# Optimization experiments

Hardware: AMD Instinct MI355X
Metric: run time of the kernel (lower is better)

Reference implementation:

```python
import jax, jax.numpy as jnp
import numpy as np

D_MODEL = 1024
D_STATE = 16
D_CONV = 4
EXPAND = 2
D_INNER = EXPAND * D_MODEL          # 2048
DT_RANK = (D_MODEL + 15) // 16      # 64
BSZ, T0, H0, W0 = 4, 8, 16, 16
SEQLEN = T0 * H0 * W0               # 2048
N_BANDS = 8


def setup_inputs() -> dict:
    key = jax.random.key(0)
    ks = jax.random.split(key, 8)
    hidden_states = jax.random.normal(ks[0], (BSZ, SEQLEN, D_MODEL), jnp.float32)
    in_proj_w = jax.random.normal(ks[1], (2 * D_INNER, D_MODEL), jnp.float32) * (D_MODEL ** -0.5)
    conv_w = jax.random.normal(ks[2], (D_INNER, 1, D_CONV), jnp.float32) * (D_CONV ** -0.5)
    conv_b = jnp.zeros((D_INNER,), jnp.float32)
    x_proj_w = jax.random.normal(ks[3], (DT_RANK + 2 * D_STATE, D_INNER), jnp.float32) * (D_INNER ** -0.5)
    dt_std = DT_RANK ** -0.5
    dt_proj_w = jax.random.uniform(ks[4], (D_INNER, DT_RANK), jnp.float32, -dt_std, dt_std)
    # inverse-softplus init of dt bias, as in the torch module
    dt = jnp.exp(jax.random.uniform(ks[5], (D_INNER,), jnp.float32)
                 * (np.log(0.1) - np.log(0.001)) + np.log(0.001))
    dt = jnp.clip(dt, 1e-4, None)
    dt_proj_b = dt + jnp.log(-jnp.expm1(-dt))
    A_log = jnp.log(jnp.tile(jnp.arange(1, D_STATE + 1, dtype=jnp.float32)[None, :], (D_INNER, 1)))
    D_param = jnp.ones((D_INNER,), jnp.float32)
    out_proj_w = jax.random.normal(ks[6], (D_MODEL, D_INNER), jnp.float32) * (D_INNER ** -0.5)
    return dict(hidden_states=hidden_states, T=T0, H=H0, W=W0,
                in_proj_w=in_proj_w, conv_w=conv_w, conv_b=conv_b,
                x_proj_w=x_proj_w, dt_proj_w=dt_proj_w, dt_proj_b=dt_proj_b,
                A_log=A_log, D=D_param, out_proj_w=out_proj_w)


def _channel_alignment(x, B, T, H, W):
    """x: (B, C, L=T*H*W) -> (align_loss scalar, features (B*T, C))."""
    C = x.shape[1]
    x4 = x.reshape(B, C, T, H, W).transpose(0, 2, 1, 3, 4).reshape(B * T, C, H, W)
    fr = jnp.fft.rfft2(x4, axes=(-2, -1))
    mag = jnp.sqrt(fr.real ** 2 + fr.imag ** 2 + 1e-8)
    mag = jnp.fft.fftshift(mag, axes=(-2, -1))
    Wr = mag.shape[-1]                      # W//2 + 1
    hg = jnp.arange(H)[:, None]
    wg = jnp.arange(Wr)[None, :]
    r = jnp.sqrt(((hg - H // 2) / H) ** 2 + ((wg - Wr // 2) / Wr) ** 2)
    masks = jnp.stack([((r >= i / N_BANDS) & (r < (i + 1) / N_BANDS)).astype(mag.dtype)
                       for i in range(N_BANDS)])          # (8, H, Wr)
    bands = jnp.einsum('bchw,khw->bck', mag, masks)        # (B*T, C, 8)
    bands = bands / (bands.sum(-1, keepdims=True) + 1e-8)
    features = bands[..., N_BANDS // 2:].sum(-1)           # (B*T, C) high-freq ratio
    fn = features / jnp.maximum(jnp.linalg.norm(features, axis=1, keepdims=True), 1e-12)
    sim = fn @ fn.T
    Bt = features.shape[0]
    loss = 1.0 - sim.sum() / (Bt * Bt)
    return loss, features


def _invert_A(A_log, features):
    """Blend A_log toward its column-flipped version, weighted by channel features."""
    A_max = A_log.max(axis=0, keepdims=True)
    A_min = A_log.min(axis=0, keepdims=True)
    A_flipped = A_max + A_min - A_log
    attention = jnp.linalg.norm(jnp.exp(A_log), axis=1)
    attention = attention / (attention.max() + 1e-8)
    f = jax.nn.softmax(jax.lax.stop_gradient(features).mean(axis=0))
    alpha = jnp.clip(f * (1.0 - attention), 0.0, 1.0)[:, None]   # (d_inner, 1)
    return (1.0 - alpha) * A_log + alpha * A_flipped


def reference(hidden_states, T, H, W, in_proj_w, conv_w, conv_b,
              x_proj_w, dt_proj_w, dt_proj_b, A_log, D, out_proj_w):
    B, L, _ = hidden_states.shape
    xz = jnp.einsum('bld,ed->bel', hidden_states, in_proj_w)      # (B, 2*d_inner, L)
    x, z = xz[:, :D_INNER], xz[:, D_INNER:]

    align_loss, features = _channel_alignment(x, B, T, H, W)
    A_log_new = _invert_A(A_log, features)
    A = -jnp.exp(A_log_new)                                       # (d_inner, d_state)

    # causal depthwise conv1d + SiLU (left pad d_conv-1 == torch pad then slice :L)
    xc = jax.lax.conv_general_dilated(x, conv_w, (1,), [(D_CONV - 1, 0)],
                                      dimension_numbers=('NCH', 'OIH', 'NCH'),
                                      feature_group_count=D_INNER)
    xc = jax.nn.silu(xc + conv_b[None, :, None])                  # (B, d_inner, L)

    x_dbl = jnp.einsum('bdl,ed->ble', xc, x_proj_w)               # (B, L, dt_rank+2N)
    dt_low = x_dbl[..., :DT_RANK]
    Bm = x_dbl[..., DT_RANK:DT_RANK + D_STATE]                    # (B, L, N)
    Cm = x_dbl[..., DT_RANK + D_STATE:]                           # (B, L, N)
    delta = jax.nn.softplus(jnp.einsum('blr,dr->bld', dt_low, dt_proj_w) + dt_proj_b)

    u = xc.transpose(0, 2, 1)                                     # (B, L, d_inner)

    def step(s, inp):
        d_t, u_t, B_t, C_t = inp                                  # (B,D),(B,D),(B,N),(B,N)
        s = s * jnp.exp(d_t[..., None] * A) + (d_t * u_t)[..., None] * B_t[:, None, :]
        y_t = jnp.einsum('bdn,bn->bd', s, C_t)
        return s, y_t

    s0 = jnp.zeros((B, D_INNER, D_STATE), delta.dtype)
    _, ys = jax.lax.scan(step, s0,
                         (delta.transpose(1, 0, 2), u.transpose(1, 0, 2),
                          Bm.transpose(1, 0, 2), Cm.transpose(1, 0, 2)))
    y = ys.transpose(1, 0, 2)                                     # (B, L, d_inner)
    y = y + u * D
    y = y * jax.nn.silu(z.transpose(0, 2, 1))
    out = jnp.einsum('bld,ed->ble', y, out_proj_w)                # (B, L, d_model)
    return out, align_loss
```

## Files before the change

kernel.cpp:

```cpp
#include <hip/hip_runtime.h>
#include <math.h>
#include <stdint.h>

#define LSEQ 2048
#define DM   1024
#define DI   2048
#define NC   32
#define CL   64

#define OFF_X     ((size_t)0)
#define OFF_Z     ((size_t)16777216)
#define OFF_U     ((size_t)33554432)
#define OFF_S     ((size_t)50331648)
#define OFF_CS    (OFF_S)
#define OFF_SDT   (OFF_S + 4194304)
#define OFF_XDBL  (OFF_S + 4456448)
#define OFF_FEAT  (OFF_S + 5242880)
#define OFF_AWS   (OFF_S + 5308448)
#define OFF_B1    ((size_t)58720256)

__device__ __forceinline__ float silu_(float x) { return x / (1.f + __expf(-x)); }
__device__ __forceinline__ float softplus_(float x) {
  return fmaxf(x, 0.f) + log1pf(__expf(-fabsf(x)));
}
__device__ __forceinline__ unsigned short f2bf(float x) {
  unsigned int u = __float_as_uint(x);
  u += 0x7fffu + ((u >> 16) & 1u);
  return (unsigned short)(u >> 16);
}
__device__ __forceinline__ float bf2f(unsigned short h) {
  return __uint_as_float(((unsigned int)h) << 16);
}

typedef __attribute__((ext_vector_type(8))) short bf16x8;
typedef __attribute__((ext_vector_type(4))) float f32x4;

__device__ __forceinline__ void gl2lds16(const void* g, void* l) {
  __builtin_amdgcn_global_load_lds(
      (const __attribute__((address_space(1))) unsigned int*)(uintptr_t)g,
      (__attribute__((address_space(3))) unsigned int*)(uintptr_t)l,
      16, 0, 0);
}

#define BARRIER_()                                   \
  do {                                               \
    asm volatile("" ::: "memory");                   \
    __builtin_amdgcn_s_barrier();                    \
    asm volatile("" ::: "memory");                   \
  } while (0)

__global__ __launch_bounds__(256) void split2_w(
    const float* __restrict__ a, unsigned short* __restrict__ oa, int ksa,
    size_t na4,
    const float* __restrict__ b, unsigned short* __restrict__ ob, int ksb)
{
  size_t i4 = ((size_t)blockIdx.x << 8) + threadIdx.x;
  const float* src; unsigned short* dst; int ks;
  if (i4 < na4) { src = a; dst = oa; ks = ksa; }
  else          { src = b; dst = ob; ks = ksb; i4 -= na4; }
  const size_t flat = i4 << 2;
  const int K = 1 << ks;
  const size_t row = flat >> ks;
  const int k = (int)(flat & (size_t)(K - 1));
  float4 v = *(const float4*)(src + flat);
  float f[4] = {v.x, v.y, v.z, v.w};
  unsigned short h[4], lo[4];
#pragma unroll
  for (int c = 0; c < 4; ++c) { h[c] = f2bf(f[c]); lo[c] = f2bf(f[c] - bf2f(h[c])); }
  unsigned short* o = dst + (row << (ks + 1)) + k;
  *(uint2*)(o)     = make_uint2((unsigned)h[0]  | ((unsigned)h[1]  << 16),
                                (unsigned)h[2]  | ((unsigned)h[3]  << 16));
  *(uint2*)(o + K) = make_uint2((unsigned)lo[0] | ((unsigned)lo[1] << 16),
                                (unsigned)lo[2] | ((unsigned)lo[3] << 16));
}

template <int NPASS, int MH, int NH>
__device__ __forceinline__ void phase_mfma(
    const unsigned short* __restrict__ shc, f32x4 (&acc)[8][4],
    int wm, int wn, int lm, int roff)
{
  bf16x8 aH[4], bH[2], aL[4], bL[2];
#pragma unroll
  for (int ii = 0; ii < 4; ++ii) {
    const int ar = (wm + (MH * 4 + ii) * 16 + lm) * 32 + roff;
    aH[ii] = *(const bf16x8*)(shc + ar);
    if constexpr (NPASS > 1) aL[ii] = *(const bf16x8*)(shc + 2 * 8192 + ar);
  }
#pragma unroll
  for (int jj = 0; jj < 2; ++jj) {
    const int br = (wn + (NH * 2 + jj) * 16 + lm) * 32 + roff;
    bH[jj] = *(const bf16x8*)(shc + 8192 + br);
    if constexpr (NPASS > 1) bL[jj] = *(const bf16x8*)(shc + 3 * 8192 + br);
  }
  __builtin_amdgcn_s_setprio(1);
#pragma unroll
  for (int ii = 0; ii < 4; ++ii)
#pragma unroll
    for (int jj = 0; jj < 2; ++jj) {
      const int i = MH * 4 + ii, j = NH * 2 + jj;
      acc[i][j] = __builtin_amdgcn_mfma_f32_16x16x32_bf16(aH[ii], bH[jj], acc[i][j], 0, 0, 0);
      if constexpr (NPASS > 1) {
        acc[i][j] = __builtin_amdgcn_mfma_f32_16x16x32_bf16(aH[ii], bL[jj], acc[i][j], 0, 0, 0);
        acc[i][j] = __builtin_amdgcn_mfma_f32_16x16x32_bf16(aL[ii], bH[jj], acc[i][j], 0, 0, 0);
      }
    }
  __builtin_amdgcn_s_setprio(0);
}

template <int NPASS>
__global__ __launch_bounds__(512, 2) void gemm_8ph(
    const unsigned short* __restrict__ Ap, const unsigned short* __restrict__ Bp,
    float* __restrict__ C, int K, int ldc)
{
  constexpr int NTEN = (NPASS > 1) ? 4 : 2;
  __shared__ unsigned short sh[2][NTEN][256 * 32];
  const int tid = threadIdx.x;
  const int bn = blockIdx.x << 8;
  const int bm = blockIdx.y << 8;
  const int K2 = K * 2;
  const int wave = tid >> 6, lane = tid & 63;
  const int wm = (wave >> 2) << 7;
  const int wn = (wave & 3) << 6;
  const int lm = lane & 15, quad = lane >> 4;
  const int roff = ((quad ^ ((lm >> 1) & 3)) << 3);

  const int r0 = tid >> 2;
  const int kq = (((tid & 3) ^ ((r0 >> 1) & 3)) << 3);
  const unsigned short* a0 = Ap + (size_t)(bm + r0) * K2 + kq;
  const unsigned short* a1 = a0 + (size_t)128 * K2;
  const unsigned short* b0 = Bp + (size_t)(bn + r0) * K2 + kq;
  const unsigned short* b1 = b0 + (size_t)128 * K2;
  const int ls0 = tid * 8, ls1 = 4096 + tid * 8;

  f32x4 acc[8][4] = {};
  const int NT = K >> 5;

  {
    unsigned short* s = &sh[0][0][0];
    gl2lds16(a0, s + ls0);
    gl2lds16(a1, s + ls1);
    if constexpr (NPASS > 1) {
      gl2lds16(a0 + K, s + 2 * 8192 + ls0);
      gl2lds16(a1 + K, s + 2 * 8192 + ls1);
    }
    gl2lds16(b0, s + 8192 + ls0);
    gl2lds16(b1, s + 8192 + ls1);
    if constexpr (NPASS > 1) {
      gl2lds16(b0 + K, s + 3 * 8192 + ls0);
      gl2lds16(b1 + K, s + 3 * 8192 + ls1);
    }
  }

  for (int t = 0; t < NT - 1; ++t) {
    const unsigned short* cur = &sh[t & 1][0][0];
    unsigned short* nxt = &sh[(t + 1) & 1][0][0];
    const int kn = (t + 1) << 5;

    gl2lds16(a0 + kn, nxt + ls0);
    gl2lds16(a1 + kn, nxt + ls1);
    if constexpr (NPASS > 1) {
      gl2lds16(a0 + K + kn, nxt + 2 * 8192 + ls0);
      gl2lds16(a1 + K + kn, nxt + 2 * 8192 + ls1);
      asm volatile("s_waitcnt vmcnt(4)" ::: "memory");
    } else {
      asm volatile("s_waitcnt vmcnt(2)" ::: "memory");
    }
    BARRIER_();
    phase_mfma<NPASS, 0, 0>(cur, acc, wm, wn, lm, roff);
    BARRIER_();
    gl2lds16(b0 + kn, nxt + 8192 + ls0);
    gl2lds16(b1 + kn, nxt + 8192 + ls1);
    if constexpr (NPASS > 1) {
      gl2lds16(b0 + K + kn, nxt + 3 * 8192 + ls0);
      gl2lds16(b1 + K + kn, nxt + 3 * 8192 + ls1);
    }
    phase_mfma<NPASS, 0, 1>(cur, acc, wm, wn, lm, roff);
    BARRIER_();
    phase_mfma<NPASS, 1, 0>(cur, acc, wm, wn, lm, roff);
    BARRIER_();
    phase_mfma<NPASS, 1, 1>(cur, acc, wm, wn, lm, roff);
    BARRIER_();
  }

  {
    const unsigned short* cur = &sh[(NT - 1) & 1][0][0];
    asm volatile("s_waitcnt vmcnt(0)" ::: "memory");
    BARRIER_();
    phase_mfma<NPASS, 0, 0>(cur, acc, wm, wn, lm, roff);
    BARRIER_();
    phase_mfma<NPASS, 0, 1>(cur, acc, wm, wn, lm, roff);
    BARRIER_();
    phase_mfma<NPASS, 1, 0>(cur, acc, wm, wn, lm, roff);
    BARRIER_();
    phase_mfma<NPASS, 1, 1>(cur, acc, wm, wn, lm, roff);
  }

#pragma unroll
  for (int i = 0; i < 8; ++i) {
    const int m = bm + wm + i * 16 + quad * 4;
#pragma unroll
    for (int j = 0; j < 4; ++j) {
      const int n = bn + wn + j * 16 + lm;
#pragma unroll
      for (int r = 0; r < 4; ++r)
        C[(size_t)(m + r) * ldc + n] = acc[i][j][r];
    }
  }
}

template <int NPASS, int A_PACKED>
__global__ __launch_bounds__(256) void gemm_mfma(
    const void* __restrict__ Avp, const unsigned short* __restrict__ Bp,
    float* __restrict__ C, int K, int ldc, int nxs)
{
  __shared__ unsigned short AsH[128 * 32];
  __shared__ unsigned short BsH[128 * 32];
  __shared__ unsigned short AsL[(NPASS > 1) ? 128 * 32 : 8];
  __shared__ unsigned short BsL[(NPASS > 1) ? 128 * 32 : 8];
  const int tid = threadIdx.x;
  const int lin = blockIdx.y * gridDim.x + blockIdx.x;
  const int xcd = lin & 7;
  const int t = lin >> 3;
  const int nmask = (1 << nxs) - 1;
  const int bn = (((t & nmask) << 3) | xcd) << 7;
  const int bm = (t >> nxs) << 7;
  const int K2 = K * 2;

  const int wave = tid >> 6, lane = tid & 63;
  const int wm = (wave >> 1) << 6, wn = (wave & 1) << 6;
  const int lm = lane & 15, quad = lane >> 4;
  const int sw = (lm >> 1) & 3;

  f32x4 acc[4][4] = {};

  const int r0 = tid >> 2;
  const int kq = ((tid & 3) ^ ((r0 >> 1) & 3)) << 3;
  const unsigned short* BgH0 = Bp + (size_t)(bn + r0) * K2 + kq;
  const unsigned short* BgH1 = Bp + (size_t)(bn + 64 + r0) * K2 + kq;
  unsigned short* lA0 = &AsH[(size_t)tid * 8];
  unsigned short* lA1 = &AsH[(size_t)(256 + tid) * 8];
  unsigned short* lB0 = &BsH[(size_t)tid * 8];
  unsigned short* lB1 = &BsH[(size_t)(256 + tid) * 8];
  unsigned short* lAl0 = (NPASS > 1) ? &AsL[(size_t)tid * 8] : nullptr;
  unsigned short* lAl1 = (NPASS > 1) ? &AsL[(size_t)(256 + tid) * 8] : nullptr;
  unsigned short* lBl0 = (NPASS > 1) ? &BsL[(size_t)tid * 8] : nullptr;
  unsigned short* lBl1 = (NPASS > 1) ? &BsL[(size_t)(256 + tid) * 8] : nullptr;

  const unsigned short* AgH0 = nullptr; const unsigned short* AgH1 = nullptr;
  const unsigned int* Apk0 = nullptr; const unsigned int* Apk1 = nullptr;
  if (A_PACKED) {
    const unsigned int* Au = (const unsigned int*)Avp;
    Apk0 = Au + (size_t)(bm + r0) * K + kq;
    Apk1 = Au + (size_t)(bm + 64 + r0) * K + kq;
  } else {
    const unsigned short* Ab = (const unsigned short*)Avp;
    AgH0 = Ab + (size_t)(bm + r0) * K2 + kq;
    AgH1 = Ab + (size_t)(bm + 64 + r0) * K2 + kq;
  }

  for (int k0 = 0; k0 < K; k0 += 32) {
    __syncthreads();
    if (A_PACKED) {
      uint4 u0 = *(const uint4*)(Apk0 + k0);
      uint4 u1 = *(const uint4*)(Apk0 + k0 + 4);
      uint4 v0 = *(const uint4*)(Apk1 + k0);
      uint4 v1 = *(const uint4*)(Apk1 + k0 + 4);
      unsigned p[8] = {u0.x, u0.y, u0.z, u0.w, u1.x, u1.y, u1.z, u1.w};
      unsigned q[8] = {v0.x, v0.y, v0.z, v0.w, v1.x, v1.y, v1.z, v1.w};
      unsigned hu[4], lu[4], hv[4], lv[4];
#pragma unroll
      for (int c = 0; c < 4; ++c) {
        hu[c] = (p[2*c] & 0xffffu) | (p[2*c+1] << 16);
        lu[c] = (p[2*c] >> 16)     | (p[2*c+1] & 0xffff0000u);
        hv[c] = (q[2*c] & 0xffffu) | (q[2*c+1] << 16);
        lv[c] = (q[2*c] >> 16)     | (q[2*c+1] & 0xffff0000u);
      }
      *(uint4*)lA0  = make_uint4(hu[0], hu[1], hu[2], hu[3]);
      *(uint4*)lA1  = make_uint4(hv[0], hv[1], hv[2], hv[3]);
      if (NPASS > 1) {
        *(uint4*)lAl0 = make_uint4(lu[0], lu[1], lu[2], lu[3]);
        *(uint4*)lAl1 = make_uint4(lv[0], lv[1], lv[2], lv[3]);
      }
    } else {
      gl2lds16(AgH0 + k0, lA0);
      gl2lds16(AgH1 + k0, lA1);
      if (NPASS > 1) {
        gl2lds16(AgH0 + K + k0, lAl0);
        gl2lds16(AgH1 + K + k0, lAl1);
      }
    }
    gl2lds16(BgH0 + k0, lB0);
    gl2lds16(BgH1 + k0, lB1);
    if (NPASS > 1) {
      gl2lds16(BgH0 + K + k0, lBl0);
      gl2lds16(BgH1 + K + k0, lBl1);
    }
    __syncthreads();

    bf16x8 aH[4], bH[4];
#pragma unroll
    for (int i = 0; i < 4; ++i)
      aH[i] = *(const bf16x8*)&AsH[(wm + i * 16 + lm) * 32 + ((quad ^ sw) << 3)];
#pragma unroll
    for (int j = 0; j < 4; ++j)
      bH[j] = *(const bf16x8*)&BsH[(wn + j * 16 + lm) * 32 + ((quad ^ sw) << 3)];
#pragma unroll
    for (int i = 0; i < 4; ++i)
#pragma unroll
      for (int j = 0; j < 4; ++j)
        acc[i][j] = __builtin_amdgcn_mfma_f32_16x16x32_bf16(aH[i], bH[j], acc[i][j], 0, 0, 0);
    if (NPASS > 1) {
      bf16x8 aL[4], bL[4];
#pragma unroll
      for (int i = 0; i < 4; ++i)
        aL[i] = *(const bf16x8*)&AsL[(wm + i * 16 + lm) * 32 + ((quad ^ sw) << 3)];
#pragma unroll
      for (int j = 0; j < 4; ++j)
        bL[j] = *(const bf16x8*)&BsL[(wn + j * 16 + lm) * 32 + ((quad ^ sw) << 3)];
#pragma unroll
      for (int i = 0; i < 4; ++i)
#pragma unroll
        for (int j = 0; j < 4; ++j) {
          acc[i][j] = __builtin_amdgcn_mfma_f32_16x16x32_bf16(aH[i], bL[j], acc[i][j], 0, 0, 0);
          acc[i][j] = __builtin_amdgcn_mfma_f32_16x16x32_bf16(aL[i], bH[j], acc[i][j], 0, 0, 0);
        }
    }
  }

#pragma unroll
  for (int i = 0; i < 4; ++i) {
    const int m = bm + wm + i * 16 + quad * 4;
#pragma unroll
    for (int j = 0; j < 4; ++j) {
      const int n = bn + wn + j * 16 + lm;
#pragma unroll
      for (int r = 0; r < 4; ++r)
        C[(size_t)(m + r) * ldc + n] = acc[i][j][r];
    }
  }
}

template <int EPI>
__global__ __launch_bounds__(256) void gemm_nt(
    const float* __restrict__ A, int lda,
    const float* __restrict__ B, int ldb,
    float* __restrict__ C, int ldc,
    int N, int K, const float* __restrict__ bias, size_t cseg)
{
  __shared__ float As[16][68];
  __shared__ float Bs[16][68];
  const int tid = threadIdx.x;
  const int bm = blockIdx.y << 6;
  const int bn = blockIdx.x << 6;
  const int kz = blockIdx.z;
  A += (size_t)kz * K;
  B += (size_t)kz * K;
  C += (size_t)kz * cseg;
  const int lr = tid >> 2;
  const int lk = (tid & 3) << 2;
  const int tx = tid & 15, ty = tid >> 4;

  float acc[4][4];
#pragma unroll
  for (int i = 0; i < 4; ++i)
#pragma unroll
    for (int j = 0; j < 4; ++j) acc[i][j] = 0.f;

  const float* Apt = A + (size_t)(bm + lr) * lda + lk;
  const float* Bpt = B + (size_t)(bn + lr) * ldb + lk;
  const bool bv = (bn + lr) < N;

  for (int k0 = 0; k0 < K; k0 += 16) {
    float4 a4 = *(const float4*)(Apt + k0);
    float4 b4 = bv ? *(const float4*)(Bpt + k0) : make_float4(0.f, 0.f, 0.f, 0.f);
    __syncthreads();
    As[lk + 0][lr] = a4.x; As[lk + 1][lr] = a4.y;
    As[lk + 2][lr] = a4.z; As[lk + 3][lr] = a4.w;
    Bs[lk + 0][lr] = b4.x; Bs[lk + 1][lr] = b4.y;
    Bs[lk + 2][lr] = b4.z; Bs[lk + 3][lr] = b4.w;
    __syncthreads();
#pragma unroll
    for (int k = 0; k < 16; ++k) {
      const float4 av = *(const float4*)(&As[k][ty << 2]);
      const float4 bw = *(const float4*)(&Bs[k][tx << 2]);
      float a4r[4] = {av.x, av.y, av.z, av.w};
      float b4r[4] = {bw.x, bw.y, bw.z, bw.w};
#pragma unroll
      for (int i = 0; i < 4; ++i)
#pragma unroll
        for (int j = 0; j < 4; ++j)
          acc[i][j] = fmaf(a4r[i], b4r[j], acc[i][j]);
    }
  }

  const int m = bm + (ty << 2);
  const int n = bn + (tx << 2);
#pragma unroll
  for (int i = 0; i < 4; ++i) {
    float v[4] = {acc[i][0], acc[i][1], acc[i][2], acc[i][3]};
    if (EPI == 1) {
#pragma unroll
      for (int j = 0; j < 4; ++j)
        if (n + j < N) v[j] = softplus_(v[j] + bias[n + j]);
    }
    if (n + 3 < N) {
      *(float4*)(C + (size_t)(m + i) * ldc + n) = make_float4(v[0], v[1], v[2], v[3]);
    } else {
#pragma unroll
      for (int j = 0; j < 4; ++j)
        if (n + j < N) C[(size_t)(m + i) * ldc + n + j] = v[j];
    }
  }
}

__global__ __launch_bounds__(256) void reduce4(
    const float* __restrict__ P, float* __restrict__ O, size_t seg)
{
  const size_t i = ((size_t)blockIdx.x << 8) + threadIdx.x;
  float4 a = ((const float4*)P)[i];
  float4 b = ((const float4*)(P + seg))[i];
  float4 c = ((const float4*)(P + 2 * seg))[i];
  float4 d = ((const float4*)(P + 3 * seg))[i];
  ((float4*)O)[i] = make_float4(a.x + b.x + c.x + d.x,
                                a.y + b.y + c.y + d.y,
                                a.z + b.z + c.z + d.z,
                                a.w + b.w + c.w + d.w);
}

__global__ __launch_bounds__(256) void feat_kernel(
    const float* __restrict__ X, float* __restrict__ features)
{
  __shared__ float xin[256][17];
  __shared__ float Rf[16 * 315];
  __shared__ float tc[16], ts[16];
  __shared__ float part2[16][16][2];

  const int tid = threadIdx.x;
  const int frame = blockIdx.x >> 7;
  const int cg = blockIdx.x & 127;
  const int b = frame >> 3, t = frame & 7;
  const int c0 = cg << 4;

  if (tid < 16) {
    float ang = 0.39269908169872414f * (float)tid;
    tc[tid] = cosf(ang);
    ts[tid] = sinf(ang);
  }
  const float* xb = X + ((size_t)(b * LSEQ + t * 256) << 11) + c0;
  for (int i = tid; i < 256 * 16; i += 256) {
    int hw = i >> 4, ci = i & 15;
    xin[hw][ci] = xb[((size_t)hw << 11) + ci];
  }
  __syncthreads();

  {
    const int ci = tid & 15, h = tid >> 4;
    float re[9], im[9];
#pragma unroll
    for (int kw = 0; kw < 9; ++kw) { re[kw] = 0.f; im[kw] = 0.f; }
#pragma unroll
    for (int w = 0; w < 16; ++w) {
      float x = xin[(h << 4) + w][ci];
#pragma unroll
      for (int kw = 0; kw < 9; ++kw) {
        int ph = (kw * w) & 15;
        re[kw] = fmaf(x, tc[ph], re[kw]);
        im[kw] = fmaf(-x, ts[ph], im[kw]);
      }
    }
#pragma unroll
    for (int kw = 0; kw < 9; ++kw) {
      Rf[ci * 315 + kw * 35 + 2 * h]     = re[kw];
      Rf[ci * 315 + kw * 35 + 2 * h + 1] = im[kw];
    }
  }
  __syncthreads();

  {
    const int ci = tid & 15, kh = tid >> 4;
    float ut = 0.f, tt = 0.f;
    for (int kw = 0; kw < 9; ++kw) {
      float fre = 0.f, fim = 0.f;
#pragma unroll
      for (int h = 0; h < 16; ++h) {
        int ph = (kh * h) & 15;
        float c = tc[ph], s = ts[ph];
        float rr = Rf[ci * 315 + kw * 35 + 2 * h];
        float ri = Rf[ci * 315 + kw * 35 + 2 * h + 1];
        fre += rr * c + ri * s;
        fim += ri * c - rr * s;
      }
      float mag = sqrtf(fre * fre + fim * fim + 1e-8f);
      int sh = (kh + 8) & 15;
      int sw2 = kw + 4; if (sw2 >= 9) sw2 -= 9;
      float dh = (float)(sh - 8) / 16.0f;
      float dw = (float)(sw2 - 4) / 9.0f;
      tt += mag;
      if (dh * dh + dw * dw >= 0.25f) ut += mag;
    }
    part2[ci][kh][0] = ut;
    part2[ci][kh][1] = tt;
  }
  __syncthreads();

  if (tid < 16) {
    float ut = 0.f, tt = 0.f;
    for (int kh = 0; kh < 16; ++kh) { ut += part2[tid][kh][0]; tt += part2[tid][kh][1]; }
    features[frame * DI + c0 + tid] = ut / (tt + 1e-8f);
  }
}

__global__ __launch_bounds__(256) void alpha_kernel(
    const float* __restrict__ feats, const float* __restrict__ A_log,
    float* __restrict__ Aws, float* __restrict__ loss_out)
{
  __shared__ float red[256];
  __shared__ float invn[32];
  __shared__ float PT[32][257];
  __shared__ float AM[256][17];
  __shared__ float sAmax[16], sAmin[16];
  const int tid = threadIdx.x;

  float pn[32];
#pragma unroll
  for (int i = 0; i < 32; ++i) pn[i] = 0.f;
  float md[8];
#pragma unroll
  for (int j = 0; j < 8; ++j) md[j] = 0.f;
  for (int i = 0; i < 32; ++i) {
#pragma unroll
    for (int j = 0; j < 8; ++j) {
      float v = feats[(i << 11) + tid + (j << 8)];
      pn[i] = fmaf(v, v, pn[i]);
      md[j] += v;
    }
  }
#pragma unroll
  for (int j = 0; j < 8; ++j) md[j] *= (1.f / 32.f);
#pragma unroll
  for (int i = 0; i < 32; ++i) PT[i][tid] = pn[i];
  __syncthreads();
  if (tid < 32) {
    float s = 0.f;
    for (int k = 0; k < 256; ++k) s += PT[tid][k];
    invn[tid] = 1.f / fmaxf(sqrtf(s), 1e-12f);
  }
  __syncthreads();

  float gsq = 0.f;
#pragma unroll
  for (int j = 0; j < 8; ++j) {
    float gd = 0.f;
    for (int i = 0; i < 32; ++i)
      gd = fmaf(feats[(i << 11) + tid + (j << 8)], invn[i], gd);
    gsq = fmaf(gd, gd, gsq);
  }
  red[tid] = gsq; __syncthreads();
  for (int s = 128; s > 0; s >>= 1) { if (tid < s) red[tid] += red[tid + s]; __syncthreads(); }
  if (tid == 0) loss_out[0] = 1.f - red[0] * (1.f / 1024.f);
  __syncthreads();

  float lm = md[0];
#pragma unroll
  for (int j = 1; j < 8; ++j) lm = fmaxf(lm, md[j]);
  red[tid] = lm; __syncthreads();
  for (int s = 128; s > 0; s >>= 1) { if (tid < s) red[tid] = fmaxf(red[tid], red[tid + s]); __syncthreads(); }
  const float mmax = red[0]; __syncthreads();

  float p[8]; float ps = 0.f;
#pragma unroll
  for (int j = 0; j < 8; ++j) { p[j] = __expf(md[j] - mmax); ps += p[j]; }
  red[tid] = ps; __syncthreads();
  for (int s = 128; s > 0; s >>= 1) { if (tid < s) red[tid] += red[tid + s]; __syncthreads(); }
  const float psum = red[0]; __syncthreads();

  float amaxl[16], aminl[16], rn[8];
#pragma unroll
  for (int n = 0; n < 16; ++n) { amaxl[n] = -1e30f; aminl[n] = 1e30f; }
#pragma unroll
  for (int j = 0; j < 8; ++j) {
    const int d = tid + (j << 8);
    float ss = 0.f;
#pragma unroll
    for (int n = 0; n < 16; ++n) {
      float a = A_log[(d << 4) + n];
      float e = __expf(a);
      ss = fmaf(e, e, ss);
      amaxl[n] = fmaxf(amaxl[n], a);
      aminl[n] = fminf(aminl[n], a);
    }
    rn[j] = sqrtf(ss);
  }
  float rm = rn[0];
#pragma unroll
  for (int j = 1; j < 8; ++j) rm = fmaxf(rm, rn[j]);
  red[tid] = rm; __syncthreads();
  for (int s = 128; s > 0; s >>= 1) { if (tid < s) red[tid] = fmaxf(red[tid], red[tid + s]); __syncthreads(); }
  const float rnmax = red[0]; __syncthreads();

#pragma unroll
  for (int n = 0; n < 16; ++n) AM[tid][n] = amaxl[n];
  __syncthreads();
  if (tid < 16) { float m = -1e30f; for (int i = 0; i < 256; ++i) m = fmaxf(m, AM[i][tid]); sAmax[tid] = m; }
  __syncthreads();
#pragma unroll
  for (int n = 0; n < 16; ++n) AM[tid][n] = aminl[n];
  __syncthreads();
  if (tid < 16) { float m = 1e30f; for (int i = 0; i < 256; ++i) m = fminf(m, AM[i][tid]); sAmin[tid] = m; }
  __syncthreads();

  const float irn = 1.f / (rnmax + 1e-8f);
#pragma unroll
  for (int j = 0; j < 8; ++j) {
    const int d = tid + (j << 8);
    const float att = rn[j] * irn;
    const float f = p[j] / psum;
    const float alpha = fminf(fmaxf(f * (1.f - att), 0.f), 1.f);
#pragma unroll
    for (int n = 0; n < 16; ++n) {
      float a = A_log[(d << 4) + n];
      float fl = sAmax[n] + sAmin[n] - a;
      float an = (1.f - alpha) * a + alpha * fl;
      Aws[(d << 4) + n] = -__expf(an) * 1.4426950408889634f;
    }
  }
}

__global__ __launch_bounds__(256) void conv_kernel(
    const float* __restrict__ X, const float* __restrict__ cw,
    const float* __restrict__ cb, float* __restrict__ U)
{
  const size_t i4 = ((size_t)blockIdx.x << 8) + threadIdx.x;
  const int e4 = (int)(i4 & 511);
  const size_t row = i4 >> 9;
  const int l = (int)(row & 2047);
  const float* xr = X + (row << 11) + (e4 << 2);
  const float4 z4 = make_float4(0.f, 0.f, 0.f, 0.f);
  float4 x0 = *(const float4*)xr;
  float4 x1 = (l >= 1) ? *(const float4*)(xr - 2048) : z4;
  float4 x2 = (l >= 2) ? *(const float4*)(xr - 4096) : z4;
  float4 x3 = (l >= 3) ? *(const float4*)(xr - 6144) : z4;
  const float4* cwf = (const float4*)cw;
  float4 bi = *(const float4*)(cb + (e4 << 2));
  float x0a[4] = {x0.x, x0.y, x0.z, x0.w};
  float x1a[4] = {x1.x, x1.y, x1.z, x1.w};
  float x2a[4] = {x2.x, x2.y, x2.z, x2.w};
  float x3a[4] = {x3.x, x3.y, x3.z, x3.w};
  float bia[4] = {bi.x, bi.y, bi.z, bi.w};
  float o[4];
#pragma unroll
  for (int c = 0; c < 4; ++c) {
    float4 w = cwf[(e4 << 2) + c];
    float acc = bia[c];
    acc = fmaf(x3a[c], w.x, acc);
    acc = fmaf(x2a[c], w.y, acc);
    acc = fmaf(x1a[c], w.z, acc);
    acc = fmaf(x0a[c], w.w, acc);
    o[c] = silu_(acc);
  }
  *(float4*)(U + (i4 << 2)) = make_float4(o[0], o[1], o[2], o[3]);
}

__global__ __launch_bounds__(256) void scan_pass1(
    const float* __restrict__ delta, const float* __restrict__ U,
    const float* __restrict__ xdbl, const float* __restrict__ Aws,
    float* __restrict__ cs, float* __restrict__ sdt)
{
  __shared__ float blds[CL * 16];
  const int tid = threadIdx.x;
  const int dg = blockIdx.x & 7;
  const int chunk = (blockIdx.x >> 3) & 31;
  const int b = blockIdx.x >> 8;
  const int d = (dg << 8) | tid;
  const int l0 = chunk * CL;

  for (int i = tid; i < CL * 16; i += 256) {
    int l = i >> 4, j = i & 15;
    blds[i] = xdbl[(size_t)(b * LSEQ + l0 + l) * 96 + 64 + j];
  }
  __syncthreads();

  float Ar[16];
#pragma unroll
  for (int n = 0; n < 16; ++n) Ar[n] = Aws[(d << 4) + n];
  float s[16];
#pragma unroll
  for (int n = 0; n < 16; ++n) s[n] = 0.f;
  float sumdt = 0.f;

  const float* dp = delta + ((size_t)b << 22) + ((size_t)l0 << 11) + d;
  const float* up = U + ((size_t)b << 22) + ((size_t)l0 << 11) + d;

  for (int l = 0; l < CL; ++l) {
    const float dt = dp[(size_t)l << 11];
    const float u = up[(size_t)l << 11];
    sumdt += dt;
    const float du = dt * u;
    const float* bl = &blds[l << 4];
#pragma unroll
    for (int n = 0; n < 16; ++n)
      s[n] = fmaf(s[n], __builtin_amdgcn_exp2f(dt * Ar[n]), du * bl[n]);
  }

  float* csp = cs + ((((size_t)b * NC + chunk) * 2048 + d) << 4);
#pragma unroll
  for (int n = 0; n < 4; ++n)
    *(float4*)(csp + (n << 2)) = make_float4(s[4*n], s[4*n+1], s[4*n+2], s[4*n+3]);
  sdt[((size_t)b * NC + chunk) * 2048 + d] = sumdt;
}

__global__ __launch_bounds__(256) void scan_mid(
    float* __restrict__ cs, const float* __restrict__ sdt,
    const float* __restrict__ Aws)
{
  const int b = blockIdx.x >> 3;
  const int d = ((blockIdx.x & 7) << 8) | threadIdx.x;
  float Ar[16];
#pragma unroll
  for (int n = 0; n < 16; ++n) Ar[n] = Aws[(d << 4) + n];
  float si[16];
#pragma unroll
  for (int n = 0; n < 16; ++n) si[n] = 0.f;

  for (int c = 0; c < NC; ++c) {
    const size_t base = ((size_t)b * NC + c) * 2048 + d;
    float* csp = cs + (base << 4);
    float sl[16];
#pragma unroll
    for (int n = 0; n < 4; ++n) {
      float4 v = *(const float4*)(csp + (n << 2));
      sl[4*n] = v.x; sl[4*n+1] = v.y; sl[4*n+2] = v.z; sl[4*n+3] = v.w;
    }
    const float sm = sdt[base];
#pragma unroll
    for (int n = 0; n < 4; ++n)
      *(float4*)(csp + (n << 2)) = make_float4(si[4*n], si[4*n+1], si[4*n+2], si[4*n+3]);
#pragma unroll
    for (int n = 0; n < 16; ++n)
      si[n] = fmaf(si[n], __builtin_amdgcn_exp2f(sm * Ar[n]), sl[n]);
  }
}

__global__ __launch_bounds__(256) void scan_pass3(
    const float* __restrict__ delta, const float* __restrict__ Z,
    float* __restrict__ U,
    const float* __restrict__ xdbl, const float* __restrict__ Aws,
    const float* __restrict__ Dp, const float* __restrict__ cs)
{
  __shared__ float bclds[CL * 32];
  const int tid = threadIdx.x;
  const int dg = blockIdx.x & 7;
  const int chunk = (blockIdx.x >> 3) & 31;
  const int b = blockIdx.x >> 8;
  const int d = (dg << 8) | tid;
  const int l0 = chunk * CL;

  for (int i = tid; i < CL * 32; i += 256) {
    int l = i >> 5, j = i & 31;
    bclds[i] = xdbl[(size_t)(b * LSEQ + l0 + l) * 96 + 64 + j];
  }
  __syncthreads();

  float Ar[16];
#pragma unroll
  for (int n = 0; n < 16; ++n) Ar[n] = Aws[(d << 4) + n];
  const float Dd = Dp[d];

  const float* csp = cs + ((((size_t)b * NC + chunk) * 2048 + d) << 4);
  float s[16];
#pragma unroll
  for (int n = 0; n < 4; ++n) {
    float4 v = *(const float4*)(csp + (n << 2));
    s[4*n] = v.x; s[4*n+1] = v.y; s[4*n+2] = v.z; s[4*n+3] = v.w;
  }

  const float* dp = delta + ((size_t)b << 22) + ((size_t)l0 << 11) + d;
  const float* zp = Z + ((size_t)b << 22) + ((size_t)l0 << 11) + d;
  float* up = U + ((size_t)b << 22) + ((size_t)l0 << 11) + d;

  for (int l = 0; l < CL; ++l) {
    const float dt = dp[(size_t)l << 11];
    const float u = up[(size_t)l << 11];
    const float z = zp[(size_t)l << 11];
    const float du = dt * u;
    const float* bcl = &bclds[l << 5];
    float y = 0.f;
#pragma unroll
    for (int n = 0; n < 16; ++n) {
      s[n] = fmaf(s[n], __builtin_amdgcn_exp2f(dt * Ar[n]), du * bcl[n]);
      y = fmaf(s[n], bcl[16 + n], y);
    }
    const float yv = fmaf(u, Dd, y);
    const float yo = yv * silu_(z);
    const unsigned short h = f2bf(yo);
    const unsigned short lo = f2bf(yo - bf2f(h));
    ((unsigned int*)up)[(size_t)l << 11] = (unsigned)h | ((unsigned)lo << 16);
  }
}

extern "C" void kernel_launch(void* const* d_in, const int* in_sizes, int n_in,
                              void* d_out, int out_size, void* d_ws, size_t ws_size,
                              hipStream_t stream)
{
  const float* hs         = (const float*)d_in[0];
  const float* in_proj_w  = (const float*)d_in[4];
  const float* conv_w     = (const float*)d_in[5];
  const float* conv_b     = (const float*)d_in[6];
  const float* x_proj_w   = (const float*)d_in[7];
  const float* dt_proj_w  = (const float*)d_in[8];
  const float* dt_proj_b  = (const float*)d_in[9];
  const float* A_log      = (const float*)d_in[10];
  const float* Dp         = (const float*)d_in[11];
  const float* out_proj_w = (const float*)d_in[12];
  float* out = (float*)d_out;
  float* ws = (float*)d_ws;

  float* X     = ws + OFF_X;
  float* Z     = ws + OFF_Z;
  float* U     = ws + OFF_U;
  float* cs    = ws + OFF_CS;
  float* sdt   = ws + OFF_SDT;
  float* xdbl  = ws + OFF_XDBL;
  float* feats = ws + OFF_FEAT;
  float* Aws   = ws + OFF_AWS;
  unsigned short* A1s = (unsigned short*)(ws + OFF_S);
  unsigned short* B1s = (unsigned short*)(ws + OFF_B1);
  unsigned short* B2s = (unsigned short*)(ws + OFF_B1);

  const dim3 blk(256);

  split2_w<<<12288, blk, 0, stream>>>(hs, A1s, 10, (size_t)2097152,
                                      in_proj_w, B1s, 10);
  gemm_8ph<3><<<dim3(8, 32), dim3(512), 0, stream>>>(A1s, B1s, X, 1024, 2048);
  gemm_8ph<1><<<dim3(8, 32), dim3(512), 0, stream>>>(A1s, B1s + (size_t)2048 * 2048, Z, 1024, 2048);
  feat_kernel<<<4096, blk, 0, stream>>>(X, feats);
  conv_kernel<<<16384, blk, 0, stream>>>(X, conv_w, conv_b, U);
  split2_w<<<2048, blk, 0, stream>>>(out_proj_w, B2s, 11, (size_t)524288,
                                     out_proj_w, B2s, 11);
  alpha_kernel<<<1, blk, 0, stream>>>(feats, A_log, Aws, out + 8388608);
  gemm_nt<0><<<dim3(2, 128, 4), blk, 0, stream>>>(U, DI, x_proj_w, DI, cs, 96, 96, 512, nullptr, (size_t)786432);
  reduce4<<<768, blk, 0, stream>>>(cs, xdbl, (size_t)786432);
  gemm_nt<1><<<dim3(32, 128, 1), blk, 0, stream>>>(xdbl, 96, dt_proj_w, 64, X, DI, DI, 64, dt_proj_b, 0);
  scan_pass1<<<1024, blk, 0, stream>>>(X, U, xdbl, Aws, cs, sdt);
  scan_mid<<<32, blk, 0, stream>>>(cs, sdt, Aws);
  scan_pass3<<<1024, blk, 0, stream>>>(X, Z, U, xdbl, Aws, Dp, cs);
  gemm_mfma<3, 1><<<dim3(8, 64), blk, 0, stream>>>(U, B2s, out, 2048, 1024, 0);
}
```

Measured before the change: 880.1 us.

## Add 512-thread packed-A GEMM for out_proj and remap block tile order

Replaces the 256-thread gemm_mfma used for the output projection with a new 512-thread kernel, gemm8_pk. It reads the A operand as packed hi/lo bf16 words, unpacks them with byte_perm in registers, and uses 256x128 tiles with async global-to-LDS double buffering. It also remaps blockIdx in gemm_8ph so blocks that run together share rows of M, which should improve L2 reuse. The aim is higher MFMA utilisation and fewer LDS bytes per tile for the last GEMM, at the cost of extra ALU work for unpacking and more register pressure.

After: 884.2 us. No clear change (+0.5%).

```diff
diff --git a/kernel.cpp b/kernel.cpp
--- a/kernel.cpp
+++ b/kernel.cpp
@@ -115,8 +115,8 @@
   constexpr int NTEN = (NPASS > 1) ? 4 : 2;
   __shared__ unsigned short sh[2][NTEN][256 * 32];
   const int tid = threadIdx.x;
-  const int bn = blockIdx.x << 8;
-  const int bm = blockIdx.y << 8;
+  const int bm = (((blockIdx.x << 2) | (blockIdx.y >> 3)) << 8);
+  const int bn = ((blockIdx.y & 7) << 8);
   const int K2 = K * 2;
   const int wave = tid >> 6, lane = tid & 63;
   const int wm = (wave >> 2) << 7;
@@ -200,6 +200,127 @@
     const int m = bm + wm + i * 16 + quad * 4;
 #pragma unroll
     for (int j = 0; j < 4; ++j) {
+      const int n = bn + wn + j * 16 + lm;
+#pragma unroll
+      for (int r = 0; r < 4; ++r)
+        C[(size_t)(m + r) * ldc + n] = acc[i][j][r];
+    }
+  }
+}
+
+template <int MH>
+__device__ __forceinline__ void phase_pk(
+    const unsigned int* __restrict__ ap,
+    const unsigned short* __restrict__ bh, const unsigned short* __restrict__ bl,
+    f32x4 (&acc)[8][2], int wm, int wn, int lm, int quad, int roffB)
+{
+  bf16x8 aH[4], aL[4], bH[2], bL[2];
+  const int sw = (lm >> 1) & 3;
+  const int Rg = (quad >> 1) * 4096;
+  const int s0 = ((2 * quad) & 3) ^ sw;
+  const int s1 = ((2 * quad + 1) & 3) ^ sw;
+#pragma unroll
+  for (int ii = 0; ii < 4; ++ii) {
+    const int r = wm + (MH * 4 + ii) * 16 + lm;
+    const uint4 w0 = *(const uint4*)(ap + Rg + ((r * 4 + s0) << 2));
+    const uint4 w1 = *(const uint4*)(ap + Rg + ((r * 4 + s1) << 2));
+    union { unsigned u[4]; bf16x8 v; } ch, cl;
+    ch.u[0] = __byte_perm(w0.x, w0.y, 0x5410u);
+    ch.u[1] = __byte_perm(w0.z, w0.w, 0x5410u);
+    ch.u[2] = __byte_perm(w1.x, w1.y, 0x5410u);
+    ch.u[3] = __byte_perm(w1.z, w1.w, 0x5410u);
+    cl.u[0] = __byte_perm(w0.x, w0.y, 0x7632u);
+    cl.u[1] = __byte_perm(w0.z, w0.w, 0x7632u);
+    cl.u[2] = __byte_perm(w1.x, w1.y, 0x7632u);
+    cl.u[3] = __byte_perm(w1.z, w1.w, 0x7632u);
+    aH[ii] = ch.v;
+    aL[ii] = cl.v;
+  }
+#pragma unroll
+  for (int jj = 0; jj < 2; ++jj) {
+    const int br = (wn + jj * 16 + lm) * 32 + roffB;
+    bH[jj] = *(const bf16x8*)(bh + br);
+    bL[jj] = *(const bf16x8*)(bl + br);
+  }
+  __builtin_amdgcn_s_setprio(1);
+#pragma unroll
+  for (int ii = 0; ii < 4; ++ii)
+#pragma unroll
+    for (int jj = 0; jj < 2; ++jj) {
+      const int i = MH * 4 + ii;
+      acc[i][jj] = __builtin_amdgcn_mfma_f32_16x16x32_bf16(aH[ii], bH[jj], acc[i][jj], 0, 0, 0);
+      acc[i][jj] = __builtin_amdgcn_mfma_f32_16x16x32_bf16(aH[ii], bL[jj], acc[i][jj], 0, 0, 0);
+      acc[i][jj] = __builtin_amdgcn_mfma_f32_16x16x32_bf16(aL[ii], bH[jj], acc[i][jj], 0, 0, 0);
+    }
+  __builtin_amdgcn_s_setprio(0);
+}
+
+__global__ __launch_bounds__(512, 2) void gemm8_pk(
+    const unsigned int* __restrict__ Ay,
+    const unsigned short* __restrict__ Bp,
+    float* __restrict__ C)
+{
+  constexpr int K = 2048, K2 = 4096, ldc = 1024, NT = 64;
+  __shared__ unsigned int   APk[2][2048 * 4];
+  __shared__ unsigned short BHs[2][128 * 32];
+  __shared__ unsigned short BLs[2][128 * 32];
+  const int tid = threadIdx.x;
+  const int bm = (((blockIdx.x << 2) | (blockIdx.y >> 3)) << 8);
+  const int bn = ((blockIdx.y & 7) << 7);
+  const int wave = tid >> 6, lane = tid & 63;
+  const int wm = (wave >> 2) << 7;
+  const int wn = (wave & 3) << 5;
+  const int lm = lane & 15, quad = lane >> 4;
+  const int roffB = ((quad ^ ((lm >> 1) & 3)) << 3);
+
+  const int ar = tid >> 2;
+  const int ko = (((tid & 3) ^ ((tid >> 3) & 3)) << 2);
+  const unsigned int* ag = Ay + (size_t)(bm + ar) * K + ko;
+
+  const int rb = tid >> 2;
+  const int kqb = (((tid & 3) ^ ((rb >> 1) & 3)) << 3);
+  const unsigned short* bg = Bp + (size_t)(bn + rb) * K2 + kqb;
+  const int lsb = tid * 8;
+
+  f32x4 acc[8][2] = {};
+
+#define STAGE_(buf, kn) do {                                                   \
+    gl2lds16(ag + (kn),                       &APk[buf][(size_t)(tid)        << 2]); \
+    gl2lds16(ag + (size_t)128 * K + (kn),     &APk[buf][(size_t)(512 + tid)  << 2]); \
+    gl2lds16(ag + 16 + (kn),                  &APk[buf][(size_t)(1024 + tid) << 2]); \
+    gl2lds16(ag + (size_t)128 * K + 16 + (kn),&APk[buf][(size_t)(1536 + tid) << 2]); \
+    gl2lds16(bg + (kn),     &BHs[buf][lsb]);                                   \
+    gl2lds16(bg + K + (kn), &BLs[buf][lsb]);                                   \
+  } while (0)
+
+  STAGE_(0, 0);
+
+  for (int t = 0; t < NT - 1; ++t) {
+    const int cb = t & 1, nb = cb ^ 1;
+    STAGE_(nb, (t + 1) << 5);
+    asm volatile("s_waitcnt vmcnt(6)" ::: "memory");
+    BARRIER_();
+    phase_pk<0>(APk[cb], BHs[cb], BLs[cb], acc, wm, wn, lm, quad, roffB);
+    BARRIER_();
+    phase_pk<1>(APk[cb], BHs[cb], BLs[cb], acc, wm, wn, lm, quad, roffB);
+    BARRIER_();
+  }
+
+  {
+    const int cb = (NT - 1) & 1;
+    asm volatile("s_waitcnt vmcnt(0)" ::: "memory");
+    BARRIER_();
+    phase_pk<0>(APk[cb], BHs[cb], BLs[cb], acc, wm, wn, lm, quad, roffB);
+    BARRIER_();
+    phase_pk<1>(APk[cb], BHs[cb], BLs[cb], acc, wm, wn, lm, quad, roffB);
+  }
+#undef STAGE_
+
+#pragma unroll
+  for (int i = 0; i < 8; ++i) {
+    const int m = bm + wm + i * 16 + quad * 4;
+#pragma unroll
+    for (int j = 0; j < 2; ++j) {
       const int n = bn + wn + j * 16 + lm;
 #pragma unroll
       for (int r = 0; r < 4; ++r)
@@ -844,5 +965,5 @@
   scan_pass1<<<1024, blk, 0, stream>>>(X, U, xdbl, Aws, cs, sdt);
   scan_mid<<<32, blk, 0, stream>>>(cs, sdt, Aws);
   scan_pass3<<<1024, blk, 0, stream>>>(X, Z, U, xdbl, Aws, Dp, cs);
-  gemm_mfma<3, 1><<<dim3(8, 64), blk, 0, stream>>>(U, B2s, out, 2048, 1024, 0);
-}
+  gemm8_pk<<<dim3(8, 32), dim3(512), 0, stream>>>((const unsigned int*)U, B2s, out);
+}
```
